# Kernel tuning notes

Measured on AMD Instinct MI355X. Metric: run time of the kernel, lower is better.

The kernel has to match this reference:

```python
import jax, jax.numpy as jnp
import numpy as np

B, S, HID = 2, 2048, 4096
H, KH, D = 32, 8, 128
WINDOW = 1024
THETA = 1000000.0


def setup_inputs() -> dict:
    key = jax.random.key(0)
    ks = jax.random.split(key, 5)
    scale = 0.02
    hidden_states = jax.random.normal(ks[0], (B, S, HID), dtype=jnp.float32)
    wq = jax.random.normal(ks[1], (HID, H * D), dtype=jnp.float32) * scale
    wk = jax.random.normal(ks[2], (HID, KH * D), dtype=jnp.float32) * scale
    wv = jax.random.normal(ks[3], (HID, KH * D), dtype=jnp.float32) * scale
    wo = jax.random.normal(ks[4], (H * D, HID), dtype=jnp.float32) * scale
    position_ids = jnp.broadcast_to(jnp.arange(S, dtype=jnp.int64 if jax.config.jax_enable_x64 else jnp.int32), (B, S))
    return {"hidden_states": hidden_states, "position_ids": position_ids,
            "wq": wq, "wk": wk, "wv": wv, "wo": wo}


def _rope_sin_cos(position_ids):
    # inv_freq over even dims, emb = concat(freqs, freqs) -> [b, s, D]
    inv_freq = 1.0 / (THETA ** (jnp.arange(0, D, 2, dtype=jnp.float32) / D))
    angles = position_ids.astype(jnp.float32)[..., None] * inv_freq  # [b, s, D/2]
    emb = jnp.concatenate([angles, angles], axis=-1)  # [b, s, D]
    return jnp.sin(emb)[:, None, :, :], jnp.cos(emb)[:, None, :, :]  # [b,1,s,D]


def _rotate_half(x):
    x1, x2 = jnp.split(x, 2, axis=-1)
    return jnp.concatenate([-x2, x1], axis=-1)


def _apply_rope(x, sin, cos):
    return x * cos + _rotate_half(x) * sin


def reference(hidden_states, position_ids, wq, wk, wv, wo):
    b, s, _ = hidden_states.shape
    # projections -> [b, heads, s, d]
    q = (hidden_states @ wq).reshape(b, s, H, D).transpose(0, 2, 1, 3)
    k = (hidden_states @ wk).reshape(b, s, KH, D).transpose(0, 2, 1, 3)
    v = (hidden_states @ wv).reshape(b, s, KH, D).transpose(0, 2, 1, 3)
    sin, cos = _rope_sin_cos(position_ids)
    q = _apply_rope(q, sin, cos)
    k = _apply_rope(k, sin, cos)
    # repeat kv heads for GQA: [b, KH, s, d] -> [b, H, s, d]
    rep = H // KH
    k = jnp.repeat(k, rep, axis=1)
    v = jnp.repeat(v, rep, axis=1)
    # sliding-window causal mask
    i = jnp.arange(s)[:, None]
    j = jnp.arange(s)[None, :]
    mask = (j <= i) & (i - j < WINDOW)  # [s, s]
    scores = jnp.einsum("bhqd,bhkd->bhqk", q, k) / jnp.sqrt(jnp.asarray(D, q.dtype))
    neg = jnp.finfo(scores.dtype).min
    scores = jnp.where(mask[None, None, :, :], scores, neg)
    attn = jax.nn.softmax(scores, axis=-1)
    out = jnp.einsum("bhqk,bhkd->bhqd", attn, v)
    out = out.transpose(0, 2, 1, 3).reshape(b, s, H * D)
    return out @ wo
```

## Files before the change

### kernel.cpp

```cpp
#include <hip/hip_runtime.h>
#include <hip/hip_bf16.h>
#include <math.h>

typedef __attribute__((ext_vector_type(8))) __bf16 bf16x8;
typedef __attribute__((ext_vector_type(4))) float f32x4;

#define MFMA16(a, b, c) __builtin_amdgcn_mfma_f32_16x16x32_bf16((a), (b), (c), 0, 0, 0)

__device__ inline void gld_lds16(const __hip_bfloat16* g, __hip_bfloat16* l) {
    __builtin_amdgcn_global_load_lds(
        (const __attribute__((address_space(1))) void*)g,
        (__attribute__((address_space(3))) void*)l, 16, 0, 0);
}

#define RAW_BARRIER() __builtin_amdgcn_s_barrier()
#define WAIT_LGKM0()                                          \
    do {                                                      \
        asm volatile("s_waitcnt lgkmcnt(0)" ::: "memory");    \
        __builtin_amdgcn_sched_barrier(0);                    \
    } while (0)
#define WAIT_VM(N) asm volatile("s_waitcnt vmcnt(" #N ")" ::: "memory")

__global__ void cast_bf16_kernel(const float* __restrict__ in, __hip_bfloat16* __restrict__ out) {
    int i = (blockIdx.x * blockDim.x + threadIdx.x) * 4;
    float4 v = *(const float4*)(in + i);
    out[i + 0] = __float2bfloat16(v.x);
    out[i + 1] = __float2bfloat16(v.y);
    out[i + 2] = __float2bfloat16(v.z);
    out[i + 3] = __float2bfloat16(v.w);
}

__global__ void transpose_cast_kernel(const float* __restrict__ w, __hip_bfloat16* __restrict__ wt,
                                      int K, int N) {
    __shared__ float tile[32][33];
    int n0 = blockIdx.x * 32, k0 = blockIdx.y * 32;
    int tx = threadIdx.x;
    int ty = threadIdx.y;
#pragma unroll
    for (int r = 0; r < 4; r++) {
        int k = k0 + ty + r * 8;
        tile[ty + r * 8][tx] = w[(size_t)k * N + n0 + tx];
    }
    __syncthreads();
#pragma unroll
    for (int r = 0; r < 4; r++) {
        int n = n0 + ty + r * 8;
        wt[(size_t)n * K + k0 + tx] = __float2bfloat16(tile[tx][ty + r * 8]);
    }
}

template <typename EPILOGUE>
__device__ __forceinline__ void gemm128_bk64(
    const __hip_bfloat16* __restrict__ A, const __hip_bfloat16* __restrict__ Bt,
    int m0, int n0, int K, __hip_bfloat16* As, __hip_bfloat16* Bs, EPILOGUE epi) {
    int tid = threadIdx.x;
    int wave = tid >> 6, lane = tid & 63;
    int l15 = lane & 15, quad = lane >> 4;

    int lr = lane >> 3;
    int c8 = (lane & 7) ^ lr;
    const __hip_bfloat16* aG = A + (size_t)(m0 + wave * 8 + lr) * K + c8 * 8;
    const __hip_bfloat16* bG = Bt + (size_t)(n0 + wave * 8 + lr) * K + c8 * 8;
    __hip_bfloat16* aL = As + wave * 512;
    __hip_bfloat16* bL = Bs + wave * 512;

    int wm = wave & 1, wn = wave >> 1;
    int e3 = l15 & 7;
    int s0 = (quad ^ e3) * 8;
    int s1 = ((4 + quad) ^ e3) * 8;
    const __hip_bfloat16* afr = As + (wm * 64 + l15) * 64;
    const __hip_bfloat16* bfr = Bs + (wn * 64 + l15) * 64;

    f32x4 acc[4][4];
#pragma unroll
    for (int mi = 0; mi < 4; mi++)
#pragma unroll
        for (int ni = 0; ni < 4; ni++) acc[mi][ni] = (f32x4){0.f, 0.f, 0.f, 0.f};

    for (int k0 = 0; k0 < K; k0 += 64) {
#pragma unroll
        for (int i = 0; i < 4; i++) {
            gld_lds16(aG + k0 + (size_t)(i * 32) * K, aL + i * 2048);
            gld_lds16(bG + k0 + (size_t)(i * 32) * K, bL + i * 2048);
        }
        __syncthreads();
        bf16x8 a0[4], b0[4], a1[4], b1[4];
#pragma unroll
        for (int mi = 0; mi < 4; mi++) {
            a0[mi] = *(const bf16x8*)(afr + mi * 1024 + s0);
            a1[mi] = *(const bf16x8*)(afr + mi * 1024 + s1);
        }
#pragma unroll
        for (int ni = 0; ni < 4; ni++) {
            b0[ni] = *(const bf16x8*)(bfr + ni * 1024 + s0);
            b1[ni] = *(const bf16x8*)(bfr + ni * 1024 + s1);
        }
#pragma unroll
        for (int mi = 0; mi < 4; mi++)
#pragma unroll
            for (int ni = 0; ni < 4; ni++) {
                acc[mi][ni] = MFMA16(a0[mi], b0[ni], acc[mi][ni]);
                acc[mi][ni] = MFMA16(a1[mi], b1[ni], acc[mi][ni]);
            }
        __syncthreads();
    }
    epi(acc, wm, wn, l15, quad);
}

__global__ __launch_bounds__(256) void gemm_qkv_kernel(
    const __hip_bfloat16* __restrict__ Xb,
    const __hip_bfloat16* __restrict__ Wt,
    __hip_bfloat16* __restrict__ Qraw,
    __hip_bfloat16* __restrict__ Kraw,
    __hip_bfloat16* __restrict__ Vtt) {
    __shared__ __hip_bfloat16 As[128 * 64];
    __shared__ __hip_bfloat16 Bs[128 * 64];
    int m0 = blockIdx.y * 128, n0 = blockIdx.x * 128;
    gemm128_bk64(Xb, Wt, m0, n0, 4096, As, Bs,
        [&](f32x4 (&acc)[4][4], int wm, int wn, int l15, int quad) {
#pragma unroll
            for (int mi = 0; mi < 4; mi++) {
#pragma unroll
                for (int ni = 0; ni < 4; ni++) {
                    int n = n0 + wn * 64 + ni * 16 + l15;
#pragma unroll
                    for (int r = 0; r < 4; r++) {
                        int m = m0 + wm * 64 + mi * 16 + quad * 4 + r;
                        int bb = m >> 11, s = m & 2047;
                        __hip_bfloat16 hv = __float2bfloat16(acc[mi][ni][r]);
                        if (n < 4096) {
                            int hh = n >> 7, d = n & 127;
                            Qraw[(((size_t)(bb * 32 + hh)) * 2048 + s) * 128 + d] = hv;
                        } else if (n < 5120) {
                            int n2 = n - 4096, hh = n2 >> 7, d = n2 & 127;
                            Kraw[(((size_t)(bb * 8 + hh)) * 2048 + s) * 128 + d] = hv;
                        } else {
                            int n2 = n - 5120, hh = n2 >> 7, d = n2 & 127;
                            Vtt[((((size_t)(bb * 8 + hh)) * 32 + (s >> 6)) * 128 + d) * 64 + (s & 63)] = hv;
                        }
                    }
                }
            }
        });
}

constexpr int TILE = 256 * 64;

template <typename EPILOGUE>
__device__ __forceinline__ void gemm256_8phase(
    const __hip_bfloat16* __restrict__ A, const __hip_bfloat16* __restrict__ Bt,
    int m0, int n0, int K, __hip_bfloat16* As, __hip_bfloat16* Bs, EPILOGUE epi) {
    int tid = threadIdx.x;
    int wave = tid >> 6, lane = tid & 63;
    int l15 = lane & 15, quad = lane >> 4;
    int wr = wave >> 2, wc = wave & 3;

    int lr = lane >> 3;
    int c8 = (lane & 7) ^ lr;
    const __hip_bfloat16* aG = A + (size_t)(m0 + wave * 8 + lr) * K + c8 * 8;
    const __hip_bfloat16* bG = Bt + (size_t)(n0 + wave * 8 + lr) * K + c8 * 8;
    int stRow = wave * 8;

    int e3 = l15 & 7;
    int s0 = (quad ^ e3) * 8;
    int s1 = ((4 + quad) ^ e3) * 8;

    f32x4 acc[8][4];
#pragma unroll
    for (int mi = 0; mi < 8; mi++)
#pragma unroll
        for (int ni = 0; ni < 4; ni++) acc[mi][ni] = (f32x4){0.f, 0.f, 0.f, 0.f};

    const int NT = K >> 6;

    auto stA = [&](int buf, int kt, int i) {
        gld_lds16(aG + (size_t)kt * 64 + (size_t)(i * 64) * K,
                  As + buf * TILE + (stRow + i * 64) * 64);
    };
    auto stB = [&](int buf, int kt, int i) {
        gld_lds16(bG + (size_t)kt * 64 + (size_t)(i * 64) * K,
                  Bs + buf * TILE + (stRow + i * 64) * 64);
    };

#pragma unroll
    for (int i = 0; i < 4; i++) stA(0, 0, i);
#pragma unroll
    for (int i = 0; i < 4; i++) stB(0, 0, i);
    {
        int k1 = (1 < NT) ? 1 : 0;
#pragma unroll
        for (int i = 0; i < 4; i++) stA(1, k1, i);
    }
    WAIT_VM(4);
    RAW_BARRIER();

    int cur = 0;
    for (int t = 0; t < NT; ++t) {
        int ktB = (t + 1 < NT) ? t + 1 : NT - 1;
        int ktA = (t + 2 < NT) ? t + 2 : NT - 1;
        const __hip_bfloat16* af = As + cur * TILE + (wr * 128 + l15) * 64;
        const __hip_bfloat16* bf = Bs + cur * TILE + (wc * 64 + l15) * 64;
        bf16x8 a0[4][2], a1[4][2], b0[2][2], b1[2][2];

#pragma unroll
        for (int mi = 0; mi < 4; mi++) {
            a0[mi][0] = *(const bf16x8*)(af + mi * 1024 + s0);
            a0[mi][1] = *(const bf16x8*)(af + mi * 1024 + s1);
        }
#pragma unroll
        for (int ni = 0; ni < 2; ni++) {
            b0[ni][0] = *(const bf16x8*)(bf + ni * 1024 + s0);
            b0[ni][1] = *(const bf16x8*)(bf + ni * 1024 + s1);
        }
        stB(cur ^ 1, ktB, 0);
        stB(cur ^ 1, ktB, 1);
        RAW_BARRIER();
        WAIT_LGKM0();
        __builtin_amdgcn_s_setprio(1);
#pragma unroll
        for (int mi = 0; mi < 4; mi++)
#pragma unroll
            for (int ni = 0; ni < 2; ni++) {
                acc[mi][ni] = MFMA16(a0[mi][0], b0[ni][0], acc[mi][ni]);
                acc[mi][ni] = MFMA16(a0[mi][1], b0[ni][1], acc[mi][ni]);
            }
        __builtin_amdgcn_s_setprio(0);
        RAW_BARRIER();

#pragma unroll
        for (int mi = 0; mi < 4; mi++) {
            a1[mi][0] = *(const bf16x8*)(af + (mi + 4) * 1024 + s0);
            a1[mi][1] = *(const bf16x8*)(af + (mi + 4) * 1024 + s1);
        }
        stB(cur ^ 1, ktB, 2);
        stB(cur ^ 1, ktB, 3);
        RAW_BARRIER();
        WAIT_LGKM0();
        __builtin_amdgcn_s_setprio(1);
#pragma unroll
        for (int mi = 0; mi < 4; mi++)
#pragma unroll
            for (int ni = 0; ni < 2; ni++) {
                acc[mi + 4][ni] = MFMA16(a1[mi][0], b0[ni][0], acc[mi + 4][ni]);
                acc[mi + 4][ni] = MFMA16(a1[mi][1], b0[ni][1], acc[mi + 4][ni]);
            }
        __builtin_amdgcn_s_setprio(0);
        RAW_BARRIER();

#pragma unroll
        for (int ni = 0; ni < 2; ni++) {
            b1[ni][0] = *(const bf16x8*)(bf + (ni + 2) * 1024 + s0);
            b1[ni][1] = *(const bf16x8*)(bf + (ni + 2) * 1024 + s1);
        }
        stA(cur, ktA, 0);
        stA(cur, ktA, 1);
        RAW_BARRIER();
        WAIT_LGKM0();
        __builtin_amdgcn_s_setprio(1);
#pragma unroll
        for (int mi = 0; mi < 4; mi++)
#pragma unroll
            for (int ni = 0; ni < 2; ni++) {
                acc[mi][ni + 2] = MFMA16(a0[mi][0], b1[ni][0], acc[mi][ni + 2]);
                acc[mi][ni + 2] = MFMA16(a0[mi][1], b1[ni][1], acc[mi][ni + 2]);
            }
        __builtin_amdgcn_s_setprio(0);
        RAW_BARRIER();

        stA(cur, ktA, 2);
        stA(cur, ktA, 3);
        RAW_BARRIER();
        __builtin_amdgcn_s_setprio(1);
#pragma unroll
        for (int mi = 0; mi < 4; mi++)
#pragma unroll
            for (int ni = 0; ni < 2; ni++) {
                acc[mi + 4][ni + 2] = MFMA16(a1[mi][0], b1[ni][0], acc[mi + 4][ni + 2]);
                acc[mi + 4][ni + 2] = MFMA16(a1[mi][1], b1[ni][1], acc[mi + 4][ni + 2]);
            }
        __builtin_amdgcn_s_setprio(0);
        WAIT_VM(4);
        RAW_BARRIER();
        cur ^= 1;
    }
    WAIT_VM(0);
    epi(acc, wr, wc, l15, quad);
}

__global__ __launch_bounds__(512, 2) void gemm_out_kernel(
    const __hip_bfloat16* __restrict__ A, const __hip_bfloat16* __restrict__ Bt,
    float* __restrict__ C) {
    __shared__ __hip_bfloat16 As[2 * TILE];
    __shared__ __hip_bfloat16 Bs[2 * TILE];
    int m0 = blockIdx.y * 256, n0 = blockIdx.x * 256;
    gemm256_8phase(A, Bt, m0, n0, 4096, As, Bs,
        [&](f32x4 (&acc)[8][4], int wr, int wc, int l15, int quad) {
            const int N = 4096;
#pragma unroll
            for (int mi = 0; mi < 8; mi++) {
#pragma unroll
                for (int ni = 0; ni < 4; ni++) {
                    int n = n0 + wc * 64 + ni * 16 + l15;
#pragma unroll
                    for (int r = 0; r < 4; r++) {
                        int m = m0 + wr * 128 + mi * 16 + quad * 4 + r;
                        C[(size_t)m * N + n] = acc[mi][ni][r];
                    }
                }
            }
        });
}

__global__ void rope_kernel(__hip_bfloat16* __restrict__ x, const int* __restrict__ pos_ids,
                            int nheads) {
    int idx = blockIdx.x * blockDim.x + threadIdx.x;
    int d = idx & 63;
    int s = (idx >> 6) & 2047;
    int bh = idx >> 17;
    int b = bh / nheads;
    float p = (float)pos_ids[b * 2048 + s];
    float inv = exp2f(-(float)d * 0.31143075889f);
    float ang = p * inv;
    float sn, cs;
    __sincosf(ang, &sn, &cs);
    size_t base = ((size_t)bh * 2048 + s) * 128;
    float x1 = __bfloat162float(x[base + d]);
    float x2 = __bfloat162float(x[base + d + 64]);
    x[base + d]      = __float2bfloat16(x1 * cs - x2 * sn);
    x[base + d + 64] = __float2bfloat16(x2 * cs + x1 * sn);
}

__global__ __launch_bounds__(256) void attn_kernel(
    const __hip_bfloat16* __restrict__ Qb, const __hip_bfloat16* __restrict__ Kb,
    const __hip_bfloat16* __restrict__ Vtt, __hip_bfloat16* __restrict__ AO) {
    const int S = 2048, D = 128;
    __shared__ __hip_bfloat16 Ks[2][64 * 128];
    __shared__ __hip_bfloat16 Vs[2][128 * 64];
    __shared__ __hip_bfloat16 Pl[4][16][72];

    int tid = threadIdx.x;
    int wave = tid >> 6, lane = tid & 63;
    int l15 = lane & 15, quad = lane >> 4;
    int base = blockIdx.x * 64;
    int i0 = base + wave * 16;
    int h = blockIdx.y, b = blockIdx.z;
    int kh = h >> 2;
    const __hip_bfloat16* Qh = Qb + (size_t)(b * 32 + h) * S * D;
    const __hip_bfloat16* Kh = Kb + (size_t)(b * 8 + kh) * S * D;
    const __hip_bfloat16* Vh = Vtt + (size_t)(b * 8 + kh) * S * D;

    bf16x8 qf[4];
    {
        const __hip_bfloat16* qrow = Qh + (size_t)(i0 + l15) * D + quad * 8;
#pragma unroll
        for (int kk = 0; kk < 4; kk++) qf[kk] = *(const bf16x8*)(qrow + kk * 32);
    }
    f32x4 o[8];
#pragma unroll
    for (int f = 0; f < 8; f++) o[f] = (f32x4){0.f, 0.f, 0.f, 0.f};
    float lrow[4] = {0.f, 0.f, 0.f, 0.f};

    int kst = (base > 1023) ? ((base - 1023) & ~63) : 0;
    const float c2 = 0.12751878882f;
    int e3 = l15 & 7;

    auto stage = [&](int key0, int buf) {
#pragma unroll
        for (int i = 0; i < 4; i++) {
            int rb = wave * 16 + i * 4;
            int row = rb + (lane >> 4);
            int c = (lane & 15) ^ (row & 7);
            gld_lds16(Kh + (size_t)(key0 + row) * 128 + c * 8, &Ks[buf][rb * 128]);
        }
        const __hip_bfloat16* Vtile = Vh + (size_t)(key0 >> 6) * (128 * 64);
#pragma unroll
        for (int i = 0; i < 4; i++) {
            int db = wave * 32 + i * 8;
            int row = db + (lane >> 3);
            int c = (lane & 7) ^ (row & 7);
            gld_lds16(Vtile + (size_t)row * 64 + c * 8, &Vs[buf][db * 64]);
        }
    };

    stage(kst, 0);

    for (int key0 = kst; key0 <= base; key0 += 64) {
        int buf = ((key0 - kst) >> 6) & 1;
        if (key0 + 64 <= base) {
            stage(key0 + 64, buf ^ 1);
            WAIT_VM(8);
        } else {
            WAIT_VM(0);
        }
        RAW_BARRIER();

        bool alive = (key0 <= i0 + 15) && (key0 + 63 >= i0 - 1023);
        if (alive) {
            f32x4 sc[4];
            __builtin_amdgcn_s_setprio(1);
#pragma unroll
            for (int kb = 0; kb < 4; kb++) {
                sc[kb] = (f32x4){0.f, 0.f, 0.f, 0.f};
                const __hip_bfloat16* krow = &Ks[buf][(kb * 16 + l15) * 128];
#pragma unroll
                for (int kk = 0; kk < 4; kk++) {
                    int slot = ((kk << 2) | quad) ^ e3;
                    bf16x8 kf = *(const bf16x8*)(krow + slot * 8);
                    sc[kb] = MFMA16(qf[kk], kf, sc[kb]);
                }
            }
            __builtin_amdgcn_s_setprio(0);
            bool interior = (key0 + 63 <= i0) && (key0 >= i0 - 1008);
            if (interior) {
#pragma unroll
                for (int kb = 0; kb < 4; kb++)
#pragma unroll
                    for (int r = 0; r < 4; r++) {
                        float p = __builtin_amdgcn_exp2f(sc[kb][r] * c2);
                        lrow[r] += p;
                        Pl[wave][quad * 4 + r][kb * 16 + l15] = __float2bfloat16(p);
                    }
            } else {
#pragma unroll
                for (int kb = 0; kb < 4; kb++)
#pragma unroll
                    for (int r = 0; r < 4; r++) {
                        int i = i0 + quad * 4 + r;
                        int j = key0 + kb * 16 + l15;
                        float v = (j <= i && i - j < 1024) ? sc[kb][r] * c2 : -1e30f;
                        float p = __builtin_amdgcn_exp2f(v);
                        lrow[r] += p;
                        Pl[wave][quad * 4 + r][kb * 16 + l15] = __float2bfloat16(p);
                    }
            }
            bf16x8 pf0 = *(const bf16x8*)(&Pl[wave][l15][quad * 8]);
            bf16x8 pf1 = *(const bf16x8*)(&Pl[wave][l15][32 + quad * 8]);
            int s0 = quad ^ e3, s1 = (4 + quad) ^ e3;
            __builtin_amdgcn_s_setprio(1);
#pragma unroll
            for (int f = 0; f < 8; f++) {
                const __hip_bfloat16* vrow = &Vs[buf][(f * 16 + l15) * 64];
                bf16x8 v0 = *(const bf16x8*)(vrow + s0 * 8);
                bf16x8 v1 = *(const bf16x8*)(vrow + s1 * 8);
                o[f] = MFMA16(pf0, v0, o[f]);
                o[f] = MFMA16(pf1, v1, o[f]);
            }
            __builtin_amdgcn_s_setprio(0);
        }
        RAW_BARRIER();
    }

#pragma unroll
    for (int r = 0; r < 4; r++) {
#pragma unroll
        for (int msk = 1; msk < 16; msk <<= 1) lrow[r] += __shfl_xor(lrow[r], msk, 64);
    }
#pragma unroll
    for (int r = 0; r < 4; r++) {
        int srow = i0 + quad * 4 + r;
        float invl = 1.f / lrow[r];
        __hip_bfloat16* orow = AO + ((size_t)(b * 2048 + srow) * 4096) + h * 128;
#pragma unroll
        for (int f = 0; f < 8; f++) orow[f * 16 + l15] = __float2bfloat16(o[f][r] * invl);
    }
}

extern "C" void kernel_launch(void* const* d_in, const int* in_sizes, int n_in,
                              void* d_out, int out_size, void* d_ws, size_t ws_size,
                              hipStream_t stream) {
    (void)in_sizes; (void)n_in; (void)out_size;
    const float* hidden = (const float*)d_in[0];
    const int* pos = (const int*)d_in[1];
    const float* wq = (const float*)d_in[2];
    const float* wk = (const float*)d_in[3];
    const float* wv = (const float*)d_in[4];
    const float* wo = (const float*)d_in[5];
    float* out = (float*)d_out;

    const int M = 4096;
    char* ws = (char*)d_ws;
    size_t off = 0;
    auto alloc = [&](size_t bytes) { char* p = ws + off; off += bytes; return p; };
    __hip_bfloat16* Xb    = (__hip_bfloat16*)alloc((size_t)M * 4096 * 2);
    __hip_bfloat16* Wqkvt = (__hip_bfloat16*)alloc((size_t)6144 * 4096 * 2);
    __hip_bfloat16* Wot   = (__hip_bfloat16*)alloc((size_t)4096 * 4096 * 2);
    __hip_bfloat16* Qb    = (__hip_bfloat16*)alloc((size_t)M * 4096 * 2);
    __hip_bfloat16* Kb    = (__hip_bfloat16*)alloc((size_t)M * 1024 * 2);
    __hip_bfloat16* Vtt   = (__hip_bfloat16*)alloc((size_t)M * 1024 * 2);
    __hip_bfloat16* AO    = (__hip_bfloat16*)alloc((size_t)M * 4096 * 2);
    if (off > ws_size) return;

    cast_bf16_kernel<<<(M * 4096) / 1024, 256, 0, stream>>>(hidden, Xb);
    dim3 tb(32, 8);
    transpose_cast_kernel<<<dim3(128, 128), tb, 0, stream>>>(wq, Wqkvt, 4096, 4096);
    transpose_cast_kernel<<<dim3(32, 128),  tb, 0, stream>>>(wk, Wqkvt + (size_t)4096 * 4096, 4096, 1024);
    transpose_cast_kernel<<<dim3(32, 128),  tb, 0, stream>>>(wv, Wqkvt + (size_t)5120 * 4096, 4096, 1024);
    transpose_cast_kernel<<<dim3(128, 128), tb, 0, stream>>>(wo, Wot, 4096, 4096);

    gemm_qkv_kernel<<<dim3(48, 32), 256, 0, stream>>>(Xb, Wqkvt, Qb, Kb, Vtt);

    rope_kernel<<<(2 * 32 * 2048 * 64) / 256, 256, 0, stream>>>(Qb, pos, 32);
    rope_kernel<<<(2 * 8 * 2048 * 64) / 256, 256, 0, stream>>>(Kb, pos, 8);

    attn_kernel<<<dim3(32, 32, 2), 256, 0, stream>>>(Qb, Kb, Vtt, AO);

    gemm_out_kernel<<<dim3(16, 16), 512, 0, stream>>>(AO, Wot, out);
}
```

Measured before the change: 809.6 us.

## Fuse RoPE into QKV GEMM epilogue and single-buffer attention with swizzled P

```diff
diff --git a/kernel.cpp b/kernel.cpp
--- a/kernel.cpp
+++ b/kernel.cpp
@@ -110,33 +110,80 @@
 __global__ __launch_bounds__(256) void gemm_qkv_kernel(
     const __hip_bfloat16* __restrict__ Xb,
     const __hip_bfloat16* __restrict__ Wt,
+    const int* __restrict__ pos,
     __hip_bfloat16* __restrict__ Qraw,
     __hip_bfloat16* __restrict__ Kraw,
     __hip_bfloat16* __restrict__ Vtt) {
-    __shared__ __hip_bfloat16 As[128 * 64];
-    __shared__ __hip_bfloat16 Bs[128 * 64];
+    __shared__ __hip_bfloat16 smem[128 * 128];
+    __hip_bfloat16* As = smem;
+    __hip_bfloat16* Bs = smem + 128 * 64;
     int m0 = blockIdx.y * 128, n0 = blockIdx.x * 128;
     gemm128_bk64(Xb, Wt, m0, n0, 4096, As, Bs,
         [&](f32x4 (&acc)[4][4], int wm, int wn, int l15, int quad) {
-#pragma unroll
-            for (int mi = 0; mi < 4; mi++) {
-#pragma unroll
-                for (int ni = 0; ni < 4; ni++) {
-                    int n = n0 + wn * 64 + ni * 16 + l15;
+            int bb = m0 >> 11;
+            if (n0 >= 5120) {
+#pragma unroll
+                for (int mi = 0; mi < 4; mi++) {
+#pragma unroll
+                    for (int ni = 0; ni < 4; ni++) {
+                        int n2 = n0 - 5120 + wn * 64 + ni * 16 + l15;
+                        int hh = n2 >> 7, d = n2 & 127;
+#pragma unroll
+                        for (int r = 0; r < 4; r++) {
+                            int m = m0 + wm * 64 + mi * 16 + quad * 4 + r;
+                            int s = m & 2047;
+                            __hip_bfloat16 hv = __float2bfloat16(acc[mi][ni][r]);
+                            Vtt[((((size_t)(bb * 8 + hh)) * 32 + (s >> 6)) * 128 + d) * 64 + (s & 63)] = hv;
+                        }
+                    }
+                }
+            } else {
+#pragma unroll
+                for (int mi = 0; mi < 4; mi++)
+#pragma unroll
+                    for (int ni = 0; ni < 4; ni++) {
+                        int nloc = wn * 64 + ni * 16 + l15;
+#pragma unroll
+                        for (int r = 0; r < 4; r++) {
+                            int mloc = wm * 64 + mi * 16 + quad * 4 + r;
+                            int ch = (nloc >> 3) ^ (mloc & 7);
+                            smem[mloc * 128 + ch * 8 + (nloc & 7)] = __float2bfloat16(acc[mi][ni][r]);
+                        }
+                    }
+                __syncthreads();
+
+                bool isQ = (n0 < 4096);
+                size_t headbase = isQ
+                    ? (size_t)(bb * 32 + (n0 >> 7)) * 2048
+                    : (size_t)(bb * 8 + ((n0 - 4096) >> 7)) * 2048;
+                __hip_bfloat16* dst = isQ ? Qraw : Kraw;
+
+                float inv4[4];
+#pragma unroll
+                for (int ni = 0; ni < 4; ni++)
+                    inv4[ni] = exp2f(-(float)(ni * 16 + l15) * 0.31143075889f);
+
+#pragma unroll
+                for (int mi = 0; mi < 4; mi++) {
 #pragma unroll
                     for (int r = 0; r < 4; r++) {
-                        int m = m0 + wm * 64 + mi * 16 + quad * 4 + r;
-                        int bb = m >> 11, s = m & 2047;
-                        __hip_bfloat16 hv = __float2bfloat16(acc[mi][ni][r]);
-                        if (n < 4096) {
-                            int hh = n >> 7, d = n & 127;
-                            Qraw[(((size_t)(bb * 32 + hh)) * 2048 + s) * 128 + d] = hv;
-                        } else if (n < 5120) {
-                            int n2 = n - 4096, hh = n2 >> 7, d = n2 & 127;
-                            Kraw[(((size_t)(bb * 8 + hh)) * 2048 + s) * 128 + d] = hv;
-                        } else {
-                            int n2 = n - 5120, hh = n2 >> 7, d = n2 & 127;
-                            Vtt[((((size_t)(bb * 8 + hh)) * 32 + (s >> 6)) * 128 + d) * 64 + (s & 63)] = hv;
+                        int mloc = wm * 64 + mi * 16 + quad * 4 + r;
+                        int s = (m0 & 2047) + mloc;
+                        float p = (float)pos[bb * 2048 + s];
+                        __hip_bfloat16* drow = dst + (headbase + s) * 128;
+#pragma unroll
+                        for (int ni = 0; ni < 4; ni++) {
+                            int nloc = wn * 64 + ni * 16 + l15;
+                            int ploc = nloc ^ 64;
+                            int pch = (ploc >> 3) ^ (mloc & 7);
+                            float partner = __bfloat162float(smem[mloc * 128 + pch * 8 + (ploc & 7)]);
+                            float own = __bfloat162float(__float2bfloat16(acc[mi][ni][r]));
+                            float ang = p * inv4[ni];
+                            float sn, cs;
+                            __sincosf(ang, &sn, &cs);
+                            float val = (nloc < 64) ? (own * cs - partner * sn)
+                                                    : (own * cs + partner * sn);
+                            drow[nloc] = __float2bfloat16(val);
                         }
                     }
                 }
@@ -311,32 +358,13 @@
         });
 }
 
-__global__ void rope_kernel(__hip_bfloat16* __restrict__ x, const int* __restrict__ pos_ids,
-                            int nheads) {
-    int idx = blockIdx.x * blockDim.x + threadIdx.x;
-    int d = idx & 63;
-    int s = (idx >> 6) & 2047;
-    int bh = idx >> 17;
-    int b = bh / nheads;
-    float p = (float)pos_ids[b * 2048 + s];
-    float inv = exp2f(-(float)d * 0.31143075889f);
-    float ang = p * inv;
-    float sn, cs;
-    __sincosf(ang, &sn, &cs);
-    size_t base = ((size_t)bh * 2048 + s) * 128;
-    float x1 = __bfloat162float(x[base + d]);
-    float x2 = __bfloat162float(x[base + d + 64]);
-    x[base + d]      = __float2bfloat16(x1 * cs - x2 * sn);
-    x[base + d + 64] = __float2bfloat16(x2 * cs + x1 * sn);
-}
-
-__global__ __launch_bounds__(256) void attn_kernel(
+__global__ __launch_bounds__(256, 4) void attn_kernel(
     const __hip_bfloat16* __restrict__ Qb, const __hip_bfloat16* __restrict__ Kb,
     const __hip_bfloat16* __restrict__ Vtt, __hip_bfloat16* __restrict__ AO) {
     const int S = 2048, D = 128;
-    __shared__ __hip_bfloat16 Ks[2][64 * 128];
-    __shared__ __hip_bfloat16 Vs[2][128 * 64];
-    __shared__ __hip_bfloat16 Pl[4][16][72];
+    __shared__ __hip_bfloat16 Ks[64 * 128];
+    __shared__ __hip_bfloat16 Vs[128 * 64];
+    __shared__ __hip_bfloat16 Pl[4][16][64];
 
     int tid = threadIdx.x;
     int wave = tid >> 6, lane = tid & 63;
@@ -364,13 +392,13 @@
     const float c2 = 0.12751878882f;
     int e3 = l15 & 7;
 
-    auto stage = [&](int key0, int buf) {
+    for (int key0 = kst; key0 <= base; key0 += 64) {
 #pragma unroll
         for (int i = 0; i < 4; i++) {
             int rb = wave * 16 + i * 4;
             int row = rb + (lane >> 4);
             int c = (lane & 15) ^ (row & 7);
-            gld_lds16(Kh + (size_t)(key0 + row) * 128 + c * 8, &Ks[buf][rb * 128]);
+            gld_lds16(Kh + (size_t)(key0 + row) * 128 + c * 8, Ks + rb * 128);
         }
         const __hip_bfloat16* Vtile = Vh + (size_t)(key0 >> 6) * (128 * 64);
 #pragma unroll
@@ -378,21 +406,9 @@
             int db = wave * 32 + i * 8;
             int row = db + (lane >> 3);
             int c = (lane & 7) ^ (row & 7);
-            gld_lds16(Vtile + (size_t)row * 64 + c * 8, &Vs[buf][db * 64]);
-        }
-    };
-
-    stage(kst, 0);
-
-    for (int key0 = kst; key0 <= base; key0 += 64) {
-        int buf = ((key0 - kst) >> 6) & 1;
-        if (key0 + 64 <= base) {
-            stage(key0 + 64, buf ^ 1);
-            WAIT_VM(8);
-        } else {
-            WAIT_VM(0);
-        }
-        RAW_BARRIER();
+            gld_lds16(Vtile + (size_t)row * 64 + c * 8, Vs + db * 64);
+        }
+        __syncthreads();
 
         bool alive = (key0 <= i0 + 15) && (key0 + 63 >= i0 - 1023);
         if (alive) {
@@ -401,7 +417,7 @@
 #pragma unroll
             for (int kb = 0; kb < 4; kb++) {
                 sc[kb] = (f32x4){0.f, 0.f, 0.f, 0.f};
-                const __hip_bfloat16* krow = &Ks[buf][(kb * 16 + l15) * 128];
+                const __hip_bfloat16* krow = Ks + (kb * 16 + l15) * 128;
 #pragma unroll
                 for (int kk = 0; kk < 4; kk++) {
                     int slot = ((kk << 2) | quad) ^ e3;
@@ -418,7 +434,8 @@
                     for (int r = 0; r < 4; r++) {
                         float p = __builtin_amdgcn_exp2f(sc[kb][r] * c2);
                         lrow[r] += p;
-                        Pl[wave][quad * 4 + r][kb * 16 + l15] = __float2bfloat16(p);
+                        int q = quad * 4 + r;
+                        Pl[wave][q][((kb * 2 + (l15 >> 3)) ^ (q & 7)) * 8 + (l15 & 7)] = __float2bfloat16(p);
                     }
             } else {
 #pragma unroll
@@ -430,16 +447,17 @@
                         float v = (j <= i && i - j < 1024) ? sc[kb][r] * c2 : -1e30f;
                         float p = __builtin_amdgcn_exp2f(v);
                         lrow[r] += p;
-                        Pl[wave][quad * 4 + r][kb * 16 + l15] = __float2bfloat16(p);
+                        int q = quad * 4 + r;
+                        Pl[wave][q][((kb * 2 + (l15 >> 3)) ^ (q & 7)) * 8 + (l15 & 7)] = __float2bfloat16(p);
                     }
             }
-            bf16x8 pf0 = *(const bf16x8*)(&Pl[wave][l15][quad * 8]);
-            bf16x8 pf1 = *(const bf16x8*)(&Pl[wave][l15][32 + quad * 8]);
+            bf16x8 pf0 = *(const bf16x8*)(&Pl[wave][l15][(quad ^ (l15 & 7)) * 8]);
+            bf16x8 pf1 = *(const bf16x8*)(&Pl[wave][l15][((4 + quad) ^ (l15 & 7)) * 8]);
             int s0 = quad ^ e3, s1 = (4 + quad) ^ e3;
             __builtin_amdgcn_s_setprio(1);
 #pragma unroll
             for (int f = 0; f < 8; f++) {
-                const __hip_bfloat16* vrow = &Vs[buf][(f * 16 + l15) * 64];
+                const __hip_bfloat16* vrow = Vs + (f * 16 + l15) * 64;
                 bf16x8 v0 = *(const bf16x8*)(vrow + s0 * 8);
                 bf16x8 v1 = *(const bf16x8*)(vrow + s1 * 8);
                 o[f] = MFMA16(pf0, v0, o[f]);
@@ -447,7 +465,7 @@
             }
             __builtin_amdgcn_s_setprio(0);
         }
-        RAW_BARRIER();
+        __syncthreads();
     }
 
 #pragma unroll
@@ -497,10 +515,7 @@
     transpose_cast_kernel<<<dim3(32, 128),  tb, 0, stream>>>(wv, Wqkvt + (size_t)5120 * 4096, 4096, 1024);
     transpose_cast_kernel<<<dim3(128, 128), tb, 0, stream>>>(wo, Wot, 4096, 4096);
 
-    gemm_qkv_kernel<<<dim3(48, 32), 256, 0, stream>>>(Xb, Wqkvt, Qb, Kb, Vtt);
-
-    rope_kernel<<<(2 * 32 * 2048 * 64) / 256, 256, 0, stream>>>(Qb, pos, 32);
-    rope_kernel<<<(2 * 8 * 2048 * 64) / 256, 256, 0, stream>>>(Kb, pos, 8);
+    gemm_qkv_kernel<<<dim3(48, 32), 256, 0, stream>>>(Xb, Wqkvt, pos, Qb, Kb, Vtt);
 
     attn_kernel<<<dim3(32, 32, 2), 256, 0, stream>>>(Qb, Kb, Vtt, AO);
 
```

Result: slower. 988.5 us (+22.1%).

## Enlarge attention query tile to 128 rows with 8 waves, drop double buffering

Applied to the files above, without the earlier changes.

```diff
diff --git a/kernel.cpp b/kernel.cpp
--- a/kernel.cpp
+++ b/kernel.cpp
@@ -330,18 +330,18 @@
     x[base + d + 64] = __float2bfloat16(x2 * cs + x1 * sn);
 }
 
-__global__ __launch_bounds__(256) void attn_kernel(
+__global__ __launch_bounds__(512, 4) void attn_kernel(
     const __hip_bfloat16* __restrict__ Qb, const __hip_bfloat16* __restrict__ Kb,
     const __hip_bfloat16* __restrict__ Vtt, __hip_bfloat16* __restrict__ AO) {
     const int S = 2048, D = 128;
-    __shared__ __hip_bfloat16 Ks[2][64 * 128];
-    __shared__ __hip_bfloat16 Vs[2][128 * 64];
-    __shared__ __hip_bfloat16 Pl[4][16][72];
+    __shared__ __hip_bfloat16 Ks[64 * 128];
+    __shared__ __hip_bfloat16 Vs[128 * 64];
+    __shared__ __hip_bfloat16 Pl[8][16][64];
 
     int tid = threadIdx.x;
     int wave = tid >> 6, lane = tid & 63;
     int l15 = lane & 15, quad = lane >> 4;
-    int base = blockIdx.x * 64;
+    int base = blockIdx.x * 128;
     int i0 = base + wave * 16;
     int h = blockIdx.y, b = blockIdx.z;
     int kh = h >> 2;
@@ -361,38 +361,27 @@
     float lrow[4] = {0.f, 0.f, 0.f, 0.f};
 
     int kst = (base > 1023) ? ((base - 1023) & ~63) : 0;
+    int kend = base + 64;
     const float c2 = 0.12751878882f;
     int e3 = l15 & 7;
 
-    auto stage = [&](int key0, int buf) {
-#pragma unroll
-        for (int i = 0; i < 4; i++) {
-            int rb = wave * 16 + i * 4;
+    for (int key0 = kst; key0 <= kend; key0 += 64) {
+#pragma unroll
+        for (int i = 0; i < 2; i++) {
+            int rb = wave * 8 + i * 4;
             int row = rb + (lane >> 4);
             int c = (lane & 15) ^ (row & 7);
-            gld_lds16(Kh + (size_t)(key0 + row) * 128 + c * 8, &Ks[buf][rb * 128]);
+            gld_lds16(Kh + (size_t)(key0 + row) * 128 + c * 8, Ks + rb * 128);
         }
         const __hip_bfloat16* Vtile = Vh + (size_t)(key0 >> 6) * (128 * 64);
 #pragma unroll
-        for (int i = 0; i < 4; i++) {
-            int db = wave * 32 + i * 8;
+        for (int i = 0; i < 2; i++) {
+            int db = wave * 16 + i * 8;
             int row = db + (lane >> 3);
             int c = (lane & 7) ^ (row & 7);
-            gld_lds16(Vtile + (size_t)row * 64 + c * 8, &Vs[buf][db * 64]);
-        }
-    };
-
-    stage(kst, 0);
-
-    for (int key0 = kst; key0 <= base; key0 += 64) {
-        int buf = ((key0 - kst) >> 6) & 1;
-        if (key0 + 64 <= base) {
-            stage(key0 + 64, buf ^ 1);
-            WAIT_VM(8);
-        } else {
-            WAIT_VM(0);
-        }
-        RAW_BARRIER();
+            gld_lds16(Vtile + (size_t)row * 64 + c * 8, Vs + db * 64);
+        }
+        __syncthreads();
 
         bool alive = (key0 <= i0 + 15) && (key0 + 63 >= i0 - 1023);
         if (alive) {
@@ -401,7 +390,7 @@
 #pragma unroll
             for (int kb = 0; kb < 4; kb++) {
                 sc[kb] = (f32x4){0.f, 0.f, 0.f, 0.f};
-                const __hip_bfloat16* krow = &Ks[buf][(kb * 16 + l15) * 128];
+                const __hip_bfloat16* krow = Ks + (kb * 16 + l15) * 128;
 #pragma unroll
                 for (int kk = 0; kk < 4; kk++) {
                     int slot = ((kk << 2) | quad) ^ e3;
@@ -418,7 +407,8 @@
                     for (int r = 0; r < 4; r++) {
                         float p = __builtin_amdgcn_exp2f(sc[kb][r] * c2);
                         lrow[r] += p;
-                        Pl[wave][quad * 4 + r][kb * 16 + l15] = __float2bfloat16(p);
+                        int q = quad * 4 + r;
+                        Pl[wave][q][((kb * 2 + (l15 >> 3)) ^ (q & 7)) * 8 + (l15 & 7)] = __float2bfloat16(p);
                     }
             } else {
 #pragma unroll
@@ -430,16 +420,17 @@
                         float v = (j <= i && i - j < 1024) ? sc[kb][r] * c2 : -1e30f;
                         float p = __builtin_amdgcn_exp2f(v);
                         lrow[r] += p;
-                        Pl[wave][quad * 4 + r][kb * 16 + l15] = __float2bfloat16(p);
+                        int q = quad * 4 + r;
+                        Pl[wave][q][((kb * 2 + (l15 >> 3)) ^ (q & 7)) * 8 + (l15 & 7)] = __float2bfloat16(p);
                     }
             }
-            bf16x8 pf0 = *(const bf16x8*)(&Pl[wave][l15][quad * 8]);
-            bf16x8 pf1 = *(const bf16x8*)(&Pl[wave][l15][32 + quad * 8]);
+            bf16x8 pf0 = *(const bf16x8*)(&Pl[wave][l15][(quad ^ (l15 & 7)) * 8]);
+            bf16x8 pf1 = *(const bf16x8*)(&Pl[wave][l15][((4 + quad) ^ (l15 & 7)) * 8]);
             int s0 = quad ^ e3, s1 = (4 + quad) ^ e3;
             __builtin_amdgcn_s_setprio(1);
 #pragma unroll
             for (int f = 0; f < 8; f++) {
-                const __hip_bfloat16* vrow = &Vs[buf][(f * 16 + l15) * 64];
+                const __hip_bfloat16* vrow = Vs + (f * 16 + l15) * 64;
                 bf16x8 v0 = *(const bf16x8*)(vrow + s0 * 8);
                 bf16x8 v1 = *(const bf16x8*)(vrow + s1 * 8);
                 o[f] = MFMA16(pf0, v0, o[f]);
@@ -447,7 +438,7 @@
             }
             __builtin_amdgcn_s_setprio(0);
         }
-        RAW_BARRIER();
+        __syncthreads();
     }
 
 #pragma unroll
@@ -502,7 +493,7 @@
     rope_kernel<<<(2 * 32 * 2048 * 64) / 256, 256, 0, stream>>>(Qb, pos, 32);
     rope_kernel<<<(2 * 8 * 2048 * 64) / 256, 256, 0, stream>>>(Kb, pos, 8);
 
-    attn_kernel<<<dim3(32, 32, 2), 256, 0, stream>>>(Qb, Kb, Vtt, AO);
+    attn_kernel<<<dim3(16, 32, 2), 512, 0, stream>>>(Qb, Kb, Vtt, AO);
 
     gemm_out_kernel<<<dim3(16, 16), 512, 0, stream>>>(AO, Wot, out);
 }
```

Result: faster. 772.0 us (-4.6%).
